# Kernel optimization log

Hardware: AMD Instinct MI355X
Metric: run time of the kernel (lower is better)

## Reference

```python
import jax, jax.numpy as jnp
import numpy as np

LN_EPS = 1e-5


def setup_inputs() -> dict:
    key = jax.random.key(0)
    k0, k1, k2, k3 = jax.random.split(key, 4)
    B, L, D = 8, 2048, 512
    x = jax.random.normal(k0, (B, L, D), dtype=jnp.float32)
    adj = jax.random.uniform(k1, (B, L, L), dtype=jnp.float32)  # non-negative dense adjacency
    pad_mask = jax.random.randint(k2, (B, L), 0, 2).astype(bool)  # True = padding position
    # learned params (dropout is identity in eval mode)
    W = jax.random.normal(k3, (D, D), dtype=jnp.float32) / np.sqrt(D)  # nn.Linear weight [out,in]
    b = jnp.zeros((D,), dtype=jnp.float32)
    ln_w = jnp.ones((D,), dtype=jnp.float32)
    ln_b = jnp.zeros((D,), dtype=jnp.float32)
    edge_weight = jnp.ones((1,), dtype=jnp.float32)
    return {"x": x, "adj": adj, "pad_mask": pad_mask, "W": W, "b": b,
            "ln_w": ln_w, "ln_b": ln_b, "edge_weight": edge_weight}


def reference(x, adj, pad_mask, W, b, ln_w, ln_b, edge_weight):
    B, L, D = x.shape
    # mask padded rows/cols, then add self-loops
    valid = (~pad_mask).astype(x.dtype)                      # [B,L]
    a = adj * valid[:, :, None] * valid[:, None, :]          # [B,L,L]
    a = a + jnp.eye(L, dtype=a.dtype)[None]
    # sym normalization D^{-1/2} A D^{-1/2} as elementwise row/col scaling
    deg = a.sum(-1)                                          # [B,L], >= 1 due to self-loops
    safe = jnp.where(deg > 0, deg, 1.0)
    dis = jnp.where(deg > 0, safe ** -0.5, 0.0)              # inf -> 0 per torch code
    a = dis[:, :, None] * a * dis[:, None, :]
    # learnable scalar edge weight, aggregate, linear, relu (dropout = identity in eval)
    agg = edge_weight[0] * jnp.einsum('blm,bmd->bld', a, x)  # [B,L,D]
    out = jax.nn.relu(agg @ W.T + b)
    out = out * (D ** -0.5)
    # residual + layernorm
    h = x + out
    mu = h.mean(-1, keepdims=True)
    var = ((h - mu) ** 2).mean(-1, keepdims=True)
    return ln_w * (h - mu) / jnp.sqrt(var + LN_EPS) + ln_b
```

## Files before the change

### kernel.cpp

```cpp
#include <hip/hip_runtime.h>

#define LN_EPS 1e-5f

typedef __attribute__((ext_vector_type(8))) short s16x8;
typedef __attribute__((ext_vector_type(4))) float f32x4;
typedef long long i64b;

__device__ inline unsigned int pk_bf16(float a, float b) {
    unsigned ua = __builtin_bit_cast(unsigned, a);
    unsigned ub = __builtin_bit_cast(unsigned, b);
    ua += 0x7fffu + ((ua >> 16) & 1u);
    ub += 0x7fffu + ((ub >> 16) & 1u);
    return (ua >> 16) | (ub & 0xffff0000u);
}
__device__ inline unsigned short cv_bf16(float a) {
    unsigned ua = __builtin_bit_cast(unsigned, a);
    ua += 0x7fffu + ((ua >> 16) & 1u);
    return (unsigned short)(ua >> 16);
}
__device__ inline float bf2f(unsigned short h) {
    unsigned u = ((unsigned)h) << 16;
    return __builtin_bit_cast(float, u);
}
__device__ inline unsigned pk2_fp8(float a, float b) {
    return (unsigned)__builtin_amdgcn_cvt_pk_fp8_f32(a, b, 0, false) & 0xffffu;
}
__device__ inline unsigned char cv_fp8(float a) {
    return (unsigned char)((unsigned)__builtin_amdgcn_cvt_pk_fp8_f32(a, 0.f, 0, false) & 0xffu);
}
__device__ inline void gl_lds16(const void* g, void* l) {
    __builtin_amdgcn_global_load_lds((const __attribute__((address_space(1))) void*)g,
                                     (__attribute__((address_space(3))) void*)l, 16, 0, 0);
}

__global__ __launch_bounds__(256) void k_scan(const int* __restrict__ pm,
                                              unsigned short* __restrict__ pos,
                                              unsigned short* __restrict__ idx,
                                              int* __restrict__ cnt, int L) {
    int b = blockIdx.x, t = threadIdx.x;
    const int* pmb = pm + (size_t)b * L;
    int j0 = t * 8;
    int v[8]; int s = 0;
    #pragma unroll
    for (int k = 0; k < 8; ++k) { v[k] = (pmb[j0 + k] == 0) ? 1 : 0; s += v[k]; }
    __shared__ int ps[256];
    ps[t] = s;
    __syncthreads();
    for (int off = 1; off < 256; off <<= 1) {
        int val = (t >= off) ? ps[t - off] : 0;
        __syncthreads();
        ps[t] += val;
        __syncthreads();
    }
    int base = ps[t] - s;
    unsigned short* posb = pos + (size_t)b * L;
    unsigned short* idxb = idx + (size_t)b * L;
    #pragma unroll
    for (int k = 0; k < 8; ++k) {
        posb[j0 + k] = (unsigned short)base;
        if (v[k]) { idxb[base] = (unsigned short)(j0 + k); base++; }
    }
    if (t == 255) cnt[b] = ps[255];
}

__global__ __launch_bounds__(256) void k_degxb(const float* __restrict__ adj,
                                               const int* __restrict__ pm,
                                               const float* __restrict__ ew,
                                               const float* __restrict__ W,
                                               const unsigned short* __restrict__ pos,
                                               const int* __restrict__ cnt,
                                               float* __restrict__ dis_o,
                                               float* __restrict__ rs,
                                               float* __restrict__ rself,
                                               unsigned char* __restrict__ amc8,
                                               const float* __restrict__ x,
                                               unsigned short* __restrict__ xb,
                                               unsigned char* __restrict__ agg8,
                                               unsigned char* __restrict__ W8,
                                               int L, int nd, int nx) {
    const int D = 512;
    int bid = blockIdx.x;
    int t = threadIdx.x;
    float e = ew[0];
    if (bid >= nd) {
        int sub = bid - nd;
        if (sub >= nx) {
            int i = ((sub - nx) * 256 + t) * 16;
            uint4 o;
            float4 v0 = *(const float4*)(W + i);
            float4 v1 = *(const float4*)(W + i + 4);
            float4 v2 = *(const float4*)(W + i + 8);
            float4 v3 = *(const float4*)(W + i + 12);
            o.x = pk2_fp8(v0.x, v0.y) | (pk2_fp8(v0.z, v0.w) << 16);
            o.y = pk2_fp8(v1.x, v1.y) | (pk2_fp8(v1.z, v1.w) << 16);
            o.z = pk2_fp8(v2.x, v2.y) | (pk2_fp8(v2.z, v2.w) << 16);
            o.w = pk2_fp8(v3.x, v3.y) | (pk2_fp8(v3.z, v3.w) << 16);
            *(uint4*)(W8 + i) = o;
            return;
        }
        int gid = sub * 256 + t;
        int row = gid >> 6;
        int co = (gid & 63) << 3;
        const float* xp = x + (size_t)row * D + co;
        float4 v0 = *(const float4*)(xp);
        float4 v1 = *(const float4*)(xp + 4);
        uint4 o;
        o.x = pk_bf16(v0.x, v0.y);
        o.y = pk_bf16(v0.z, v0.w);
        o.z = pk_bf16(v1.x, v1.y);
        o.w = pk_bf16(v1.z, v1.w);
        *(uint4*)(xb + (size_t)row * D + co) = o;
        if (pm[row] != 0) {
            uint2 oa;
            oa.x = pk2_fp8(e * v0.x, e * v0.y) | (pk2_fp8(e * v0.z, e * v0.w) << 16);
            oa.y = pk2_fp8(e * v1.x, e * v1.y) | (pk2_fp8(e * v1.z, e * v1.w) << 16);
            *(uint2*)(agg8 + (size_t)row * D + co) = oa;
        }
        return;
    }
    int row = bid;
    int b = row / L;
    int i = row - b * L;
    const int* pmb = pm + (size_t)b * L;
    if (pmb[i] != 0) {
        if (t == 0) { dis_o[row] = 1.f; rs[row] = 0.f; rself[row] = e; }
        return;
    }
    __shared__ __align__(16) unsigned char ls8[2048 + 16];
    __shared__ float wsum[4];
    const float* arow = adj + (size_t)row * L;
    const unsigned short* posb = pos + (size_t)b * L;
    int rloc = posb[i];
    int cb = cnt[b];
    int kcap = (cb + 63) & ~63;

    for (int k = cb + t; k < kcap; k += 256) ls8[k] = 0;

    int j0 = t * 8;
    float4 a0 = *(const float4*)(arow + j0);
    float4 a1 = *(const float4*)(arow + j0 + 4);
    int4 p0 = *(const int4*)(pmb + j0);
    int4 p1 = *(const int4*)(pmb + j0 + 4);
    uint4 pv = *(const uint4*)(posb + j0);
    unsigned pc0 = pv.x & 0xffffu, pc1 = pv.x >> 16;
    unsigned pc2 = pv.y & 0xffffu, pc3 = pv.y >> 16;
    unsigned pc4 = pv.z & 0xffffu, pc5 = pv.z >> 16;
    unsigned pc6 = pv.w & 0xffffu, pc7 = pv.w >> 16;
    float m0 = p0.x == 0 ? a0.x : 0.f;
    float m1 = p0.y == 0 ? a0.y : 0.f;
    float m2 = p0.z == 0 ? a0.z : 0.f;
    float m3 = p0.w == 0 ? a0.w : 0.f;
    float m4 = p1.x == 0 ? a1.x : 0.f;
    float m5 = p1.y == 0 ? a1.y : 0.f;
    float m6 = p1.z == 0 ? a1.z : 0.f;
    float m7 = p1.w == 0 ? a1.w : 0.f;
    float s = ((m0 + m1) + (m2 + m3)) + ((m4 + m5) + (m6 + m7));
    if (p0.x == 0) ls8[pc0] = cv_fp8(m0);
    if (p0.y == 0) ls8[pc1] = cv_fp8(m1);
    if (p0.z == 0) ls8[pc2] = cv_fp8(m2);
    if (p0.w == 0) ls8[pc3] = cv_fp8(m3);
    if (p1.x == 0) ls8[pc4] = cv_fp8(m4);
    if (p1.y == 0) ls8[pc5] = cv_fp8(m5);
    if (p1.z == 0) ls8[pc6] = cv_fp8(m6);
    if (p1.w == 0) ls8[pc7] = cv_fp8(m7);

    #pragma unroll
    for (int off = 32; off; off >>= 1) s += __shfl_down(s, off);
    if ((t & 63) == 0) wsum[t >> 6] = s;
    __syncthreads();

    unsigned char* amrow = amc8 + ((size_t)b * L + rloc) * L;
    int j0b = t * 8;
    if (j0b < kcap) *(uint2*)(amrow + j0b) = *(const uint2*)(ls8 + j0b);

    if (t == 0) {
        float tot = wsum[0] + wsum[1] + wsum[2] + wsum[3];
        float d = rsqrtf(1.f + tot);
        dis_o[row]  = d;
        rs[row]     = e * d;
        rself[row]  = e * d * d;
    }
}

__global__ __launch_bounds__(256) void k_yt(const unsigned short* __restrict__ xb,
                                            const float* __restrict__ dis,
                                            const unsigned short* __restrict__ idx,
                                            const int* __restrict__ cnt,
                                            unsigned char* __restrict__ yc8,
                                            int L, int D) {
    int b = blockIdx.z;
    int kb = blockIdx.x << 6;
    int db = blockIdx.y << 6;
    int cb = cnt[b];
    if (kb >= cb) return;
    __shared__ float tile[64][65];
    int t = threadIdx.x;
    int kk = t >> 2, c4 = (t & 3) << 4;
    int kg = kb + kk;
    if (kg < cb) {
        int ol = idx[(size_t)b * L + kg];
        float dl = dis[(size_t)b * L + ol];
        const unsigned short* xp = xb + ((size_t)b * L + ol) * D + db + c4;
        uint4 h0 = *(const uint4*)(xp);
        uint4 h1 = *(const uint4*)(xp + 8);
        unsigned hv[8] = {h0.x, h0.y, h0.z, h0.w, h1.x, h1.y, h1.z, h1.w};
        #pragma unroll
        for (int k = 0; k < 8; ++k) {
            tile[kk][c4 + 2 * k + 0] = bf2f((unsigned short)(hv[k] & 0xffffu)) * dl;
            tile[kk][c4 + 2 * k + 1] = bf2f((unsigned short)(hv[k] >> 16)) * dl;
        }
    } else {
        #pragma unroll
        for (int k = 0; k < 16; ++k) tile[kk][c4 + k] = 0.f;
    }
    __syncthreads();
    int dr = t >> 2, k0 = (t & 3) << 4;
    unsigned char* op = yc8 + ((size_t)b * D + db + dr) * L + kb + k0;
    uint4 o;
    o.x = pk2_fp8(tile[k0 + 0][dr],  tile[k0 + 1][dr])  | (pk2_fp8(tile[k0 + 2][dr],  tile[k0 + 3][dr])  << 16);
    o.y = pk2_fp8(tile[k0 + 4][dr],  tile[k0 + 5][dr])  | (pk2_fp8(tile[k0 + 6][dr],  tile[k0 + 7][dr])  << 16);
    o.z = pk2_fp8(tile[k0 + 8][dr],  tile[k0 + 9][dr])  | (pk2_fp8(tile[k0 + 10][dr], tile[k0 + 11][dr]) << 16);
    o.w = pk2_fp8(tile[k0 + 12][dr], tile[k0 + 13][dr]) | (pk2_fp8(tile[k0 + 14][dr], tile[k0 + 15][dr]) << 16);
    *(uint4*)(op) = o;
}

__global__ __launch_bounds__(256) void k_aggmm(
    const unsigned char* __restrict__ amc8,
    const unsigned char* __restrict__ yc8,
    const unsigned short* __restrict__ xb,
    const float* __restrict__ rs,
    const float* __restrict__ rself,
    const unsigned short* __restrict__ idx,
    const int* __restrict__ cnt,
    unsigned char* __restrict__ agg8,
    int L, int D)
{
    __shared__ __align__(16) unsigned char As[64 * 64];
    __shared__ __align__(16) unsigned char Bs[128 * 64];
    int bid = blockIdx.x;
    int wid = (bid & 7) * 128 + (bid >> 3);
    int b   = wid >> 7;
    int t6  = wid & 127;
    int brow = (t6 >> 2) << 6;
    int bcol = (t6 & 3) << 7;

    int Mc = cnt[b];
    if (brow >= Mc) return;
    int Kc = (Mc + 63) & ~63;

    int t = threadIdx.x;
    int lane = t & 63;
    int w = t >> 6;
    int wr = ((w >> 1) & 1) << 5;
    int wc = (w & 1) << 6;

    const unsigned char* amb = amc8 + ((size_t)b * L + brow) * L;
    const unsigned char* yb  = yc8 + ((size_t)b * D + bcol) * L;
    const unsigned short* idxb = idx + (size_t)b * L;

    int r4 = t >> 2;
    int c4 = t & 3;

    f32x4 acc[2][4];
    #pragma unroll
    for (int i = 0; i < 2; ++i)
        #pragma unroll
        for (int j = 0; j < 4; ++j)
            acc[i][j] = (f32x4){0.f, 0.f, 0.f, 0.f};

    const int lane15 = lane & 15;
    const int k8 = (lane >> 4) << 3;

    for (int kc = 0; kc < Kc; kc += 64) {
        {
            int sc = c4 ^ (r4 & 3);
            gl_lds16(amb + (size_t)r4 * L + kc + sc * 16, As + r4 * 64 + c4 * 16);
        }
        #pragma unroll
        for (int q = 0; q < 2; ++q) {
            int row = (q << 6) + r4;
            int sc = c4 ^ (row & 3);
            gl_lds16(yb + (size_t)row * L + kc + sc * 16, Bs + row * 64 + c4 * 16);
        }
        asm volatile("s_waitcnt vmcnt(0)" ::: "memory");
        __syncthreads();
        #pragma unroll
        for (int kk = 0; kk < 2; ++kk) {
            i64b af[2], bg[4];
            #pragma unroll
            for (int f = 0; f < 2; ++f) {
                int ar = wr + (f << 4) + lane15;
                af[f] = *(const i64b*)(As + ar * 64 + (((kk << 5) + k8) ^ ((ar & 3) << 4)));
            }
            #pragma unroll
            for (int f = 0; f < 4; ++f) {
                int br = wc + (f << 4) + lane15;
                bg[f] = *(const i64b*)(Bs + br * 64 + (((kk << 5) + k8) ^ ((br & 3) << 4)));
            }
            #pragma unroll
            for (int fm = 0; fm < 2; ++fm)
                #pragma unroll
                for (int fn = 0; fn < 4; ++fn)
                    acc[fm][fn] = __builtin_amdgcn_mfma_f32_16x16x32_fp8_fp8(af[fm], bg[fn], acc[fm][fn], 0, 0, 0);
        }
        __syncthreads();
    }

    int col = lane15;
    int r0 = (lane >> 4) << 2;
    size_t bL = (size_t)b * L;
    #pragma unroll
    for (int fm = 0; fm < 2; ++fm) {
        #pragma unroll
        for (int j = 0; j < 4; ++j) {
            int rcmp = brow + wr + (fm << 4) + r0 + j;
            if (rcmp < Mc) {
                int gi = idxb[rcmp];
                float rsi = rs[bL + gi];
                float rfi = rself[bL + gi];
                const unsigned short* xrow = xb + (bL + gi) * (size_t)D;
                unsigned char* orow = agg8 + (bL + gi) * (size_t)D;
                #pragma unroll
                for (int fn = 0; fn < 4; ++fn) {
                    int gd = bcol + wc + (fn << 4) + col;
                    float v = rsi * acc[fm][fn][j] + rfi * bf2f(xrow[gd]);
                    orow[gd] = cv_fp8(v);
                }
            }
        }
    }
}

__global__ __launch_bounds__(256) void k_linln(
    const unsigned char* __restrict__ agg8,
    const unsigned char* __restrict__ W8,
    const float* __restrict__ bias,
    const unsigned short* __restrict__ xb,
    const float* __restrict__ lnw,
    const float* __restrict__ lnb,
    float* __restrict__ out)
{
    const int D = 512;
    __shared__ __align__(16) unsigned char As[32 * 64];
    __shared__ __align__(16) unsigned char Bs[512 * 64];
    __shared__ float psum[32][4], psq[32][4];

    int i0 = blockIdx.x << 5;
    int t = threadIdx.x;
    int lane = t & 63;
    int w = t >> 6;
    int wcol = w << 7;

    int r4 = t >> 2;
    int c4 = t & 3;

    f32x4 acc[2][8];
    #pragma unroll
    for (int i = 0; i < 2; ++i)
        #pragma unroll
        for (int j = 0; j < 8; ++j)
            acc[i][j] = (f32x4){0.f, 0.f, 0.f, 0.f};

    const int lane15 = lane & 15;
    const int k8 = (lane >> 4) << 3;

    for (int kc = 0; kc < D; kc += 64) {
        if (t < 128) {
            int row = t >> 2;
            int sc = c4 ^ (row & 3);
            gl_lds16(agg8 + (size_t)(i0 + row) * D + kc + sc * 16, As + t * 16);
        }
        #pragma unroll
        for (int q = 0; q < 8; ++q) {
            int row = (q << 6) + r4;
            int sc = c4 ^ (row & 3);
            gl_lds16(W8 + (size_t)row * D + kc + sc * 16, Bs + row * 64 + c4 * 16);
        }
        asm volatile("s_waitcnt vmcnt(0)" ::: "memory");
        __syncthreads();
        #pragma unroll
        for (int kk = 0; kk < 2; ++kk) {
            i64b af[2], bg[8];
            #pragma unroll
            for (int f = 0; f < 2; ++f) {
                int ar = (f << 4) + lane15;
                af[f] = *(const i64b*)(As + ar * 64 + (((kk << 5) + k8) ^ ((ar & 3) << 4)));
            }
            #pragma unroll
            for (int f = 0; f < 8; ++f) {
                int br = wcol + (f << 4) + lane15;
                bg[f] = *(const i64b*)(Bs + br * 64 + (((kk << 5) + k8) ^ ((br & 3) << 4)));
            }
            #pragma unroll
            for (int fm = 0; fm < 2; ++fm)
                #pragma unroll
                for (int fn = 0; fn < 8; ++fn)
                    acc[fm][fn] = __builtin_amdgcn_mfma_f32_16x16x32_fp8_fp8(af[fm], bg[fn], acc[fm][fn], 0, 0, 0);
        }
        __syncthreads();
    }

    const float scale = 0.044194173824159216f;
    float bi[8], lw[8], lb[8];
    #pragma unroll
    for (int fn = 0; fn < 8; ++fn) {
        int colg = wcol + (fn << 4) + lane15;
        bi[fn] = bias[colg];
        lw[fn] = lnw[colg];
        lb[fn] = lnb[colg];
    }
    int r0 = (lane >> 4) << 2;
    #pragma unroll
    for (int fm = 0; fm < 2; ++fm) {
        #pragma unroll
        for (int j = 0; j < 4; ++j) {
            int r = (fm << 4) + r0 + j;
            const unsigned short* xrow = xb + (size_t)(i0 + r) * D;
            float s = 0.f, q = 0.f;
            #pragma unroll
            for (int fn = 0; fn < 8; ++fn) {
                int colg = wcol + (fn << 4) + lane15;
                float v = fmaxf(acc[fm][fn][j] + bi[fn], 0.f) * scale + bf2f(xrow[colg]);
                acc[fm][fn][j] = v;
                s += v;
                q += v * v;
            }
            #pragma unroll
            for (int m = 1; m < 16; m <<= 1) {
                s += __shfl_xor(s, m);
                q += __shfl_xor(q, m);
            }
            if (lane15 == 0) { psum[r][w] = s; psq[r][w] = q; }
        }
    }
    __syncthreads();
    #pragma unroll
    for (int fm = 0; fm < 2; ++fm) {
        #pragma unroll
        for (int j = 0; j < 4; ++j) {
            int r = (fm << 4) + r0 + j;
            float s = psum[r][0] + psum[r][1] + psum[r][2] + psum[r][3];
            float q = psq[r][0] + psq[r][1] + psq[r][2] + psq[r][3];
            float mu = s * (1.f / 512.f);
            float var = q * (1.f / 512.f) - mu * mu;
            float rstd = rsqrtf(var + LN_EPS);
            float* orow = out + (size_t)(i0 + r) * D;
            #pragma unroll
            for (int fn = 0; fn < 8; ++fn) {
                int colg = wcol + (fn << 4) + lane15;
                orow[colg] = lw[fn] * (acc[fm][fn][j] - mu) * rstd + lb[fn];
            }
        }
    }
}

extern "C" void kernel_launch(void* const* d_in, const int* in_sizes, int n_in,
                              void* d_out, int out_size, void* d_ws, size_t ws_size,
                              hipStream_t stream) {
    const float* x    = (const float*)d_in[0];
    const float* adj  = (const float*)d_in[1];
    const int*   pm   = (const int*)d_in[2];
    const float* W    = (const float*)d_in[3];
    const float* bias = (const float*)d_in[4];
    const float* lnw  = (const float*)d_in[5];
    const float* lnb  = (const float*)d_in[6];
    const float* ew   = (const float*)d_in[7];

    int BL = in_sizes[2];
    int L  = in_sizes[1] / BL;
    int B  = BL / L;
    int D  = in_sizes[0] / BL;

    char* ws = (char*)d_ws;
    size_t off = 0;
    float* dis   = (float*)(ws + off); off += (size_t)BL * 4;
    float* rs    = (float*)(ws + off); off += (size_t)BL * 4;
    float* rself = (float*)(ws + off); off += (size_t)BL * 4;
    unsigned short* pos = (unsigned short*)(ws + off); off += (size_t)BL * 2;
    unsigned short* idx = (unsigned short*)(ws + off); off += (size_t)BL * 2;
    int* cnt = (int*)(ws + off); off += 64;
    unsigned char* amc8 = (unsigned char*)(ws + off); off += (size_t)BL * L;
    unsigned char* yc8  = (unsigned char*)(ws + off); off += (size_t)BL * D;
    unsigned char* W8   = (unsigned char*)(ws + off); off += (size_t)D * D;
    unsigned char* agg8 = (unsigned char*)(ws + off); off += (size_t)BL * D;
    unsigned short* xb  = (unsigned short*)(ws + off); off += (size_t)BL * D * 2;

    float* out = (float*)d_out;
    int nx = (BL * D) / (256 * 8);
    int nw = (D * D) / (256 * 16);

    k_scan<<<B, 256, 0, stream>>>(pm, pos, idx, cnt, L);
    k_degxb<<<BL + nx + nw, 256, 0, stream>>>(adj, pm, ew, W, pos, cnt,
                                              dis, rs, rself, amc8, x, xb, agg8, W8, L, BL, nx);
    k_yt<<<dim3(L / 64, D / 64, B), 256, 0, stream>>>(xb, dis, idx, cnt, yc8, L, D);
    k_aggmm<<<B * (L / 64) * (D / 128), 256, 0, stream>>>(amc8, yc8, xb, rs, rself, idx, cnt, agg8, L, D);
    k_linln<<<BL / 32, 256, 0, stream>>>(agg8, W8, bias, xb, lnw, lnb, out);
}
```

Baseline: 84.39 us.

## Fold prefix scan into degree kernel and halve aggregation GEMM row tile

Removes the separate k_scan launch: every row block of k_degxb now recomputes the per-batch prefix sum over the padding mask in shared memory and derives its compacted row position itself. The block whose compacted position is zero writes the idx list and the count. Separately, the aggregation GEMM tile drops from 64 to 32 rows, which doubles the grid and halves accumulators per thread, trading B-tile reuse for more parallelism. The redundant per-row scan adds roughly a dozen barriers and extra mask loads to each of the BL row blocks.

```diff
diff --git a/kernel.cpp b/kernel.cpp
--- a/kernel.cpp
+++ b/kernel.cpp
@@ -13,11 +13,6 @@
     ub += 0x7fffu + ((ub >> 16) & 1u);
     return (ua >> 16) | (ub & 0xffff0000u);
 }
-__device__ inline unsigned short cv_bf16(float a) {
-    unsigned ua = __builtin_bit_cast(unsigned, a);
-    ua += 0x7fffu + ((ua >> 16) & 1u);
-    return (unsigned short)(ua >> 16);
-}
 __device__ inline float bf2f(unsigned short h) {
     unsigned u = ((unsigned)h) << 16;
     return __builtin_bit_cast(float, u);
@@ -31,44 +26,14 @@
 __device__ inline void gl_lds16(const void* g, void* l) {
     __builtin_amdgcn_global_load_lds((const __attribute__((address_space(1))) void*)g,
                                      (__attribute__((address_space(3))) void*)l, 16, 0, 0);
-}
-
-__global__ __launch_bounds__(256) void k_scan(const int* __restrict__ pm,
-                                              unsigned short* __restrict__ pos,
-                                              unsigned short* __restrict__ idx,
-                                              int* __restrict__ cnt, int L) {
-    int b = blockIdx.x, t = threadIdx.x;
-    const int* pmb = pm + (size_t)b * L;
-    int j0 = t * 8;
-    int v[8]; int s = 0;
-    #pragma unroll
-    for (int k = 0; k < 8; ++k) { v[k] = (pmb[j0 + k] == 0) ? 1 : 0; s += v[k]; }
-    __shared__ int ps[256];
-    ps[t] = s;
-    __syncthreads();
-    for (int off = 1; off < 256; off <<= 1) {
-        int val = (t >= off) ? ps[t - off] : 0;
-        __syncthreads();
-        ps[t] += val;
-        __syncthreads();
-    }
-    int base = ps[t] - s;
-    unsigned short* posb = pos + (size_t)b * L;
-    unsigned short* idxb = idx + (size_t)b * L;
-    #pragma unroll
-    for (int k = 0; k < 8; ++k) {
-        posb[j0 + k] = (unsigned short)base;
-        if (v[k]) { idxb[base] = (unsigned short)(j0 + k); base++; }
-    }
-    if (t == 255) cnt[b] = ps[255];
 }
 
 __global__ __launch_bounds__(256) void k_degxb(const float* __restrict__ adj,
                                                const int* __restrict__ pm,
                                                const float* __restrict__ ew,
                                                const float* __restrict__ W,
-                                               const unsigned short* __restrict__ pos,
-                                               const int* __restrict__ cnt,
+                                               int* __restrict__ cnt,
+                                               unsigned short* __restrict__ idx,
                                                float* __restrict__ dis_o,
                                                float* __restrict__ rs,
                                                float* __restrict__ rself,
@@ -127,51 +92,75 @@
         return;
     }
     __shared__ __align__(16) unsigned char ls8[2048 + 16];
+    __shared__ int ps[256];
     __shared__ float wsum[4];
+    __shared__ int rloc_sh;
     const float* arow = adj + (size_t)row * L;
-    const unsigned short* posb = pos + (size_t)b * L;
-    int rloc = posb[i];
-    int cb = cnt[b];
+
+    int j0 = t * 8;
+    int4 p0 = *(const int4*)(pmb + j0);
+    int4 p1 = *(const int4*)(pmb + j0 + 4);
+    int v[8];
+    v[0] = (p0.x == 0); v[1] = (p0.y == 0); v[2] = (p0.z == 0); v[3] = (p0.w == 0);
+    v[4] = (p1.x == 0); v[5] = (p1.y == 0); v[6] = (p1.z == 0); v[7] = (p1.w == 0);
+    int s8 = v[0] + v[1] + v[2] + v[3] + v[4] + v[5] + v[6] + v[7];
+    ps[t] = s8;
+    __syncthreads();
+    for (int off = 1; off < 256; off <<= 1) {
+        int val = (t >= off) ? ps[t - off] : 0;
+        __syncthreads();
+        ps[t] += val;
+        __syncthreads();
+    }
+    int base = ps[t] - s8;
+    int cb = ps[255];
     int kcap = (cb + 63) & ~63;
+    if (t == (i >> 3)) {
+        int c = ps[t] - s8;
+        int ii = i & 7;
+        #pragma unroll
+        for (int k = 0; k < 8; ++k) if (k < ii) c += v[k];
+        rloc_sh = c;
+    }
 
     for (int k = cb + t; k < kcap; k += 256) ls8[k] = 0;
 
-    int j0 = t * 8;
     float4 a0 = *(const float4*)(arow + j0);
     float4 a1 = *(const float4*)(arow + j0 + 4);
-    int4 p0 = *(const int4*)(pmb + j0);
-    int4 p1 = *(const int4*)(pmb + j0 + 4);
-    uint4 pv = *(const uint4*)(posb + j0);
-    unsigned pc0 = pv.x & 0xffffu, pc1 = pv.x >> 16;
-    unsigned pc2 = pv.y & 0xffffu, pc3 = pv.y >> 16;
-    unsigned pc4 = pv.z & 0xffffu, pc5 = pv.z >> 16;
-    unsigned pc6 = pv.w & 0xffffu, pc7 = pv.w >> 16;
-    float m0 = p0.x == 0 ? a0.x : 0.f;
-    float m1 = p0.y == 0 ? a0.y : 0.f;
-    float m2 = p0.z == 0 ? a0.z : 0.f;
-    float m3 = p0.w == 0 ? a0.w : 0.f;
-    float m4 = p1.x == 0 ? a1.x : 0.f;
-    float m5 = p1.y == 0 ? a1.y : 0.f;
-    float m6 = p1.z == 0 ? a1.z : 0.f;
-    float m7 = p1.w == 0 ? a1.w : 0.f;
-    float s = ((m0 + m1) + (m2 + m3)) + ((m4 + m5) + (m6 + m7));
-    if (p0.x == 0) ls8[pc0] = cv_fp8(m0);
-    if (p0.y == 0) ls8[pc1] = cv_fp8(m1);
-    if (p0.z == 0) ls8[pc2] = cv_fp8(m2);
-    if (p0.w == 0) ls8[pc3] = cv_fp8(m3);
-    if (p1.x == 0) ls8[pc4] = cv_fp8(m4);
-    if (p1.y == 0) ls8[pc5] = cv_fp8(m5);
-    if (p1.z == 0) ls8[pc6] = cv_fp8(m6);
-    if (p1.w == 0) ls8[pc7] = cv_fp8(m7);
+    float m[8];
+    m[0] = v[0] ? a0.x : 0.f;
+    m[1] = v[1] ? a0.y : 0.f;
+    m[2] = v[2] ? a0.z : 0.f;
+    m[3] = v[3] ? a0.w : 0.f;
+    m[4] = v[4] ? a1.x : 0.f;
+    m[5] = v[5] ? a1.y : 0.f;
+    m[6] = v[6] ? a1.z : 0.f;
+    m[7] = v[7] ? a1.w : 0.f;
+    float s = ((m[0] + m[1]) + (m[2] + m[3])) + ((m[4] + m[5]) + (m[6] + m[7]));
+    {
+        int pc = base;
+        #pragma unroll
+        for (int k = 0; k < 8; ++k)
+            if (v[k]) { ls8[pc] = cv_fp8(m[k]); pc++; }
+    }
 
     #pragma unroll
     for (int off = 32; off; off >>= 1) s += __shfl_down(s, off);
     if ((t & 63) == 0) wsum[t >> 6] = s;
     __syncthreads();
 
+    int rloc = rloc_sh;
     unsigned char* amrow = amc8 + ((size_t)b * L + rloc) * L;
-    int j0b = t * 8;
-    if (j0b < kcap) *(uint2*)(amrow + j0b) = *(const uint2*)(ls8 + j0b);
+    if (j0 < kcap) *(uint2*)(amrow + j0) = *(const uint2*)(ls8 + j0);
+
+    if (rloc == 0) {
+        unsigned short* idxb = idx + (size_t)b * L;
+        int bb = base;
+        #pragma unroll
+        for (int k = 0; k < 8; ++k)
+            if (v[k]) { idxb[bb] = (unsigned short)(j0 + k); bb++; }
+        if (t == 255) cnt[b] = cb;
+    }
 
     if (t == 0) {
         float tot = wsum[0] + wsum[1] + wsum[2] + wsum[3];
@@ -235,13 +224,13 @@
     unsigned char* __restrict__ agg8,
     int L, int D)
 {
-    __shared__ __align__(16) unsigned char As[64 * 64];
+    __shared__ __align__(16) unsigned char As[32 * 64];
     __shared__ __align__(16) unsigned char Bs[128 * 64];
     int bid = blockIdx.x;
-    int wid = (bid & 7) * 128 + (bid >> 3);
-    int b   = wid >> 7;
-    int t6  = wid & 127;
-    int brow = (t6 >> 2) << 6;
+    int wid = (bid & 7) * 256 + (bid >> 3);
+    int b   = wid >> 8;
+    int t6  = wid & 255;
+    int brow = (t6 >> 2) << 5;
     int bcol = (t6 & 3) << 7;
 
     int Mc = cnt[b];
@@ -251,7 +240,7 @@
     int t = threadIdx.x;
     int lane = t & 63;
     int w = t >> 6;
-    int wr = ((w >> 1) & 1) << 5;
+    int wr = ((w >> 1) & 1) << 4;
     int wc = (w & 1) << 6;
 
     const unsigned char* amb = amc8 + ((size_t)b * L + brow) * L;
@@ -261,36 +250,33 @@
     int r4 = t >> 2;
     int c4 = t & 3;
 
-    f32x4 acc[2][4];
-    #pragma unroll
-    for (int i = 0; i < 2; ++i)
-        #pragma unroll
-        for (int j = 0; j < 4; ++j)
-            acc[i][j] = (f32x4){0.f, 0.f, 0.f, 0.f};
+    f32x4 acc[4];
+    #pragma unroll
+    for (int j = 0; j < 4; ++j) acc[j] = (f32x4){0.f, 0.f, 0.f, 0.f};
 
     const int lane15 = lane & 15;
     const int k8 = (lane >> 4) << 3;
 
     for (int kc = 0; kc < Kc; kc += 64) {
-        {
-            int sc = c4 ^ (r4 & 3);
-            gl_lds16(amb + (size_t)r4 * L + kc + sc * 16, As + r4 * 64 + c4 * 16);
+        if (t < 128) {
+            int rowa = t >> 2;
+            int sc = c4 ^ (rowa & 3);
+            gl_lds16(amb + (size_t)rowa * L + kc + sc * 16, As + t * 16);
         }
         #pragma unroll
         for (int q = 0; q < 2; ++q) {
-            int row = (q << 6) + r4;
-            int sc = c4 ^ (row & 3);
-            gl_lds16(yb + (size_t)row * L + kc + sc * 16, Bs + row * 64 + c4 * 16);
+            int rowb = (q << 6) + r4;
+            int sc = c4 ^ (rowb & 3);
+            gl_lds16(yb + (size_t)rowb * L + kc + sc * 16, Bs + rowb * 64 + c4 * 16);
         }
         asm volatile("s_waitcnt vmcnt(0)" ::: "memory");
         __syncthreads();
         #pragma unroll
         for (int kk = 0; kk < 2; ++kk) {
-            i64b af[2], bg[4];
-            #pragma unroll
-            for (int f = 0; f < 2; ++f) {
-                int ar = wr + (f << 4) + lane15;
-                af[f] = *(const i64b*)(As + ar * 64 + (((kk << 5) + k8) ^ ((ar & 3) << 4)));
+            i64b af, bg[4];
+            {
+                int ar = wr + lane15;
+                af = *(const i64b*)(As + ar * 64 + (((kk << 5) + k8) ^ ((ar & 3) << 4)));
             }
             #pragma unroll
             for (int f = 0; f < 4; ++f) {
@@ -298,10 +284,8 @@
                 bg[f] = *(const i64b*)(Bs + br * 64 + (((kk << 5) + k8) ^ ((br & 3) << 4)));
             }
             #pragma unroll
-            for (int fm = 0; fm < 2; ++fm)
-                #pragma unroll
-                for (int fn = 0; fn < 4; ++fn)
-                    acc[fm][fn] = __builtin_amdgcn_mfma_f32_16x16x32_fp8_fp8(af[fm], bg[fn], acc[fm][fn], 0, 0, 0);
+            for (int fn = 0; fn < 4; ++fn)
+                acc[fn] = __builtin_amdgcn_mfma_f32_16x16x32_fp8_fp8(af, bg[fn], acc[fn], 0, 0, 0);
         }
         __syncthreads();
     }
@@ -310,22 +294,19 @@
     int r0 = (lane >> 4) << 2;
     size_t bL = (size_t)b * L;
     #pragma unroll
-    for (int fm = 0; fm < 2; ++fm) {
-        #pragma unroll
-        for (int j = 0; j < 4; ++j) {
-            int rcmp = brow + wr + (fm << 4) + r0 + j;
-            if (rcmp < Mc) {
-                int gi = idxb[rcmp];
-                float rsi = rs[bL + gi];
-                float rfi = rself[bL + gi];
-                const unsigned short* xrow = xb + (bL + gi) * (size_t)D;
-                unsigned char* orow = agg8 + (bL + gi) * (size_t)D;
-                #pragma unroll
-                for (int fn = 0; fn < 4; ++fn) {
-                    int gd = bcol + wc + (fn << 4) + col;
-                    float v = rsi * acc[fm][fn][j] + rfi * bf2f(xrow[gd]);
-                    orow[gd] = cv_fp8(v);
-                }
+    for (int j = 0; j < 4; ++j) {
+        int rcmp = brow + wr + r0 + j;
+        if (rcmp < Mc) {
+            int gi = idxb[rcmp];
+            float rsi = rs[bL + gi];
+            float rfi = rself[bL + gi];
+            const unsigned short* xrow = xb + (bL + gi) * (size_t)D;
+            unsigned char* orow = agg8 + (bL + gi) * (size_t)D;
+            #pragma unroll
+            for (int fn = 0; fn < 4; ++fn) {
+                int gd = bcol + wc + (fn << 4) + col;
+                float v = rsi * acc[fn][j] + rfi * bf2f(xrow[gd]);
+                orow[gd] = cv_fp8(v);
             }
         }
     }
@@ -476,7 +457,6 @@
     float* dis   = (float*)(ws + off); off += (size_t)BL * 4;
     float* rs    = (float*)(ws + off); off += (size_t)BL * 4;
     float* rself = (float*)(ws + off); off += (size_t)BL * 4;
-    unsigned short* pos = (unsigned short*)(ws + off); off += (size_t)BL * 2;
     unsigned short* idx = (unsigned short*)(ws + off); off += (size_t)BL * 2;
     int* cnt = (int*)(ws + off); off += 64;
     unsigned char* amc8 = (unsigned char*)(ws + off); off += (size_t)BL * L;
@@ -489,10 +469,9 @@
     int nx = (BL * D) / (256 * 8);
     int nw = (D * D) / (256 * 16);
 
-    k_scan<<<B, 256, 0, stream>>>(pm, pos, idx, cnt, L);
-    k_degxb<<<BL + nx + nw, 256, 0, stream>>>(adj, pm, ew, W, pos, cnt,
+    k_degxb<<<BL + nx + nw, 256, 0, stream>>>(adj, pm, ew, W, cnt, idx,
                                               dis, rs, rself, amc8, x, xb, agg8, W8, L, BL, nx);
     k_yt<<<dim3(L / 64, D / 64, B), 256, 0, stream>>>(xb, dis, idx, cnt, yc8, L, D);
-    k_aggmm<<<B * (L / 64) * (D / 128), 256, 0, stream>>>(amc8, yc8, xb, rs, rself, idx, cnt, agg8, L, D);
+    k_aggmm<<<B * (L / 32) * (D / 128), 256, 0, stream>>>(amc8, yc8, xb, rs, rself, idx, cnt, agg8, L, D);
     k_linln<<<BL / 32, 256, 0, stream>>>(agg8, W8, bias, xb, lnw, lnb, out);
 }
```

New measurement: 85.65 us. Within noise of the previous version (+1.5%).
